# Optimization experiments

Hardware: AMD Instinct MI355X
Metric: run time of the kernel (lower is better)

Reference implementation:

```python
import jax, jax.numpy as jnp
import numpy as np

BETA = 0.25


def setup_inputs() -> dict:
    key = jax.random.key(0)
    k1, k2 = jax.random.split(key)
    x = jax.random.normal(k1, (64, 32, 32, 64), dtype=jnp.float32)
    # codebook stored as [embedding_dim, num_embeddings], as in the layer
    embeddings = jax.random.normal(k2, (64, 1024), dtype=jnp.float32) * 0.05
    return {"x": x, "embeddings": embeddings}


def reference(x, embeddings):
    input_shape = x.shape
    d = embeddings.shape[0]
    flat = x.reshape(-1, d)  # [N, D]

    sim = flat @ embeddings  # [N, K]
    distances = (
        jnp.sum(flat ** 2, axis=1, keepdims=True)
        + jnp.sum(embeddings ** 2, axis=0)
        - 2.0 * sim
    )
    encoding_indices = jnp.argmin(distances, axis=1)  # [N]

    # one_hot @ embeddings.T is mathematically a gather of codebook rows
    quantized = jnp.take(embeddings.T, encoding_indices, axis=0)  # [N, D]
    quantized = quantized.reshape(input_shape)

    commitment_loss = jnp.mean((jax.lax.stop_gradient(quantized) - x) ** 2)
    codebook_loss = jnp.mean((quantized - jax.lax.stop_gradient(x)) ** 2)
    loss = BETA * commitment_loss + codebook_loss

    # straight-through estimator
    quantized_st = x + jax.lax.stop_gradient(quantized - x)
    return quantized_st, loss
```

## Files before the change

kernel.cpp:

```cpp
#include <hip/hip_runtime.h>

#define D 64
#define K 1024
#define NPTS 65536
#define OUT_ELEMS (NPTS * D)
#define PAD4 17

typedef __bf16 bf16x8 __attribute__((ext_vector_type(8)));
typedef float  f32x4  __attribute__((ext_vector_type(4)));


static __device__ __forceinline__ void split1(float v, __bf16& h, __bf16& mid,
                                              __bf16& lo) {
    h = (__bf16)v;
    const float fh = (float)h;
    const float r1 = v - fh;
    mid = (__bf16)r1;
    const float fm = (float)mid;
    lo = (__bf16)(r1 - fm);
}

__global__ __launch_bounds__(256) void vq_prep(const float* __restrict__ emb,
                                               float* __restrict__ eT,
                                               float* __restrict__ enorm_h,
                                               __bf16* __restrict__ ebh,
                                               __bf16* __restrict__ ebm,
                                               __bf16* __restrict__ ebl,
                                               float* __restrict__ loss_out) {
    __shared__ float tile[64][65];
    const int t    = threadIdx.x;
    const int lane = t & 63;
    const int quad = t >> 6;
    const int k0   = blockIdx.x * 64;

#pragma unroll
    for (int i = 0; i < 16; ++i) {
        const int d = i * 4 + quad;
        tile[d][lane] = emb[d * K + k0 + lane];
    }
    __syncthreads();

    const int kk = t >> 2, c = t & 3;
    const int krow = k0 + kk;
#pragma unroll
    for (int j = 0; j < 16; ++j) {
        const int d = c * 16 + j;
        const float v = tile[d][kk];
        const int idx = krow * D + d;
        eT[idx] = v;
        __bf16 h, mid, lo;
        split1(v, h, mid, lo);
        ebh[idx] = h; ebm[idx] = mid; ebl[idx] = lo;
    }

    if (t < 64) {
        float s = __fmul_rn(tile[0][t], tile[0][t]);
        for (int dd = 1; dd < D; ++dd)
            s = __fadd_rn(s, __fmul_rn(tile[dd][t], tile[dd][t]));
        enorm_h[k0 + t] = 0.5f * s;
    }
    if (blockIdx.x == 0 && t == 0) *loss_out = 0.0f;
}

static __device__ __forceinline__ float sq8(float a, float b, float c, float d,
                                            float e, float f, float g, float h) {
    float r = __fmul_rn(a, a);
    r = __fadd_rn(r, __fmul_rn(b, b));
    r = __fadd_rn(r, __fmul_rn(c, c));
    r = __fadd_rn(r, __fmul_rn(d, d));
    r = __fadd_rn(r, __fmul_rn(e, e));
    r = __fadd_rn(r, __fmul_rn(f, f));
    r = __fadd_rn(r, __fmul_rn(g, g));
    r = __fadd_rn(r, __fmul_rn(h, h));
    return r;
}

#define PINF(v) asm volatile("" : "+v"(v))

#define MFMA(A, B, C) C = __builtin_amdgcn_mfma_f32_16x16x32_bf16(A, B, C, 0, 0, 0)

#define MKFRAG(FH, FM, FL, U0, U1) {                      \
    __bf16 h_, m_, l_;                                    \
    split1(U0.x, h_, m_, l_); FH[0]=h_; FM[0]=m_; FL[0]=l_; \
    split1(U0.y, h_, m_, l_); FH[1]=h_; FM[1]=m_; FL[1]=l_; \
    split1(U0.z, h_, m_, l_); FH[2]=h_; FM[2]=m_; FL[2]=l_; \
    split1(U0.w, h_, m_, l_); FH[3]=h_; FM[3]=m_; FL[3]=l_; \
    split1(U1.x, h_, m_, l_); FH[4]=h_; FM[4]=m_; FL[4]=l_; \
    split1(U1.y, h_, m_, l_); FH[5]=h_; FM[5]=m_; FL[5]=l_; \
    split1(U1.z, h_, m_, l_); FH[6]=h_; FM[6]=m_; FL[6]=l_; \
    split1(U1.w, h_, m_, l_); FH[7]=h_; FM[7]=m_; FL[7]=l_; }

static __device__ __forceinline__ void cp16(const void* gptr, void* lptr) {
    __builtin_amdgcn_global_load_lds(
        (const __attribute__((address_space(1))) void*)gptr,
        (__attribute__((address_space(3))) void*)lptr, 16, 0, 0);
}

__global__ __launch_bounds__(512, 4) void vq_main(const float* __restrict__ x,
        const float* __restrict__ eT, const float* __restrict__ enorm_h,
        const __bf16* __restrict__ ebh, const __bf16* __restrict__ ebm,
        const __bf16* __restrict__ ebl,
        float* __restrict__ out, float* __restrict__ loss_out) {
    __shared__ __align__(16) char smem[51712];
    float*  rpart = (float*)(smem + 12288);
    int*    swin  = (int*)(smem + 16384);
    float*  skey  = (float*)(smem + 16896);
    int*    sct   = (int*)(smem + 25088);
    float4* slab  = (float4*)(smem + 16896);

    const int t     = threadIdx.x;
    const int lane  = t & 63;
    const int w     = t >> 6;
    const int m     = lane & 15;
    const int quad  = lane >> 4;
    const int pbase = blockIdx.x * 128 + w * 16;

    const int n0   = lane >> 3;
    const int jj   = lane & 7;
    const int soff = n0 * 128 + (((jj - n0) & 7) << 4);
    const char* gsA = (w < 2) ? (const char*)ebh
                    : (w < 4) ? (const char*)ebm : (const char*)ebl;
    const int   IA  = w & 1;
    const int   dA  = (w >> 1) * 2048 + IA * 1024;
    const int   sA  = soff + IA * 1024;

    const int o0 = (m * 8 + ((quad + m) & 7)) * 16;
    const int o1 = (m * 8 + ((4 + quad + m) & 7)) * 16;

    if (w < 6) cp16(gsA + sA, smem + dA);

    bf16x8 Ah0, Am0, Al0, Ah1, Am1, Al1;
#define LOADA(HH, FH, FM, FL) {                                            \
    const float* px = x + ((size_t)(pbase + m)) * D + HH * 32 + quad * 8;  \
    const float4 u0 = *(const float4*)px;                                  \
    const float4 u1 = *(const float4*)(px + 4);                            \
    rpart[(w * 16 + m) * 8 + (HH * 4 + quad)] =                            \
        sq8(u0.x, u0.y, u0.z, u0.w, u1.x, u1.y, u1.z, u1.w);               \
    MKFRAG(FH, FM, FL, u0, u1); }
    LOADA(0, Ah0, Am0, Al0)
    LOADA(1, Ah1, Am1, Al1)
#undef LOADA
    PINF(Ah0); PINF(Am0); PINF(Al0); PINF(Ah1); PINF(Am1); PINF(Al1);

    const float FINF = 3.402823466e38f;
    float bk0 = FINF, bk1 = FINF, bk2 = FINF, bk3 = FINF;
    int   bc0 = 0, bc1 = 0, bc2 = 0, bc3 = 0;

#define TILE_BODY(BBOFF, CT, PRET, PREOFF) {                               \
    __syncthreads();   \
    if (w < 6) cp16(gsA + (size_t)(PRET) * 2048 + sA, smem + (PREOFF) + dA); \
    const char* bb = smem + (BBOFF);                                       \
    const bf16x8 Bh0 = *(const bf16x8*)(bb + o0);                          \
    const bf16x8 Bh1 = *(const bf16x8*)(bb + o1);                          \
    const bf16x8 Bm0 = *(const bf16x8*)(bb + 2048 + o0);                   \
    const bf16x8 Bm1 = *(const bf16x8*)(bb + 2048 + o1);                   \
    const bf16x8 Bl0 = *(const bf16x8*)(bb + 4096 + o0);                   \
    const bf16x8 Bl1 = *(const bf16x8*)(bb + 4096 + o1);                   \
    const float enh = enorm_h[(CT) * 16 + m];                              \
    f32x4 ca = {0.f,0.f,0.f,0.f}, cb = {0.f,0.f,0.f,0.f};                  \
    MFMA(Ah0, Bh0, ca); MFMA(Ah1, Bh1, cb);                        \
    MFMA(Am0, Bh0, ca); MFMA(Am1, Bh1, cb);                        \
    MFMA(Ah0, Bm0, ca); MFMA(Ah1, Bm1, cb);                        \
    MFMA(Am0, Bm0, ca); MFMA(Am1, Bm1, cb);                        \
    MFMA(Ah0, Bl0, ca); MFMA(Ah1, Bl1, cb);                        \
    MFMA(Al0, Bh0, ca); MFMA(Al1, Bh1, cb);                        \
    const f32x4 c0 = ca + cb;                                              \
    { const float kv = enh - c0[0]; if (kv < bk0) { bk0 = kv; bc0 = (CT); } } \
    { const float kv = enh - c0[1]; if (kv < bk1) { bk1 = kv; bc1 = (CT); } } \
    { const float kv = enh - c0[2]; if (kv < bk2) { bk2 = kv; bc2 = (CT); } } \
    { const float kv = enh - c0[3]; if (kv < bk3) { bk3 = kv; bc3 = (CT); } } }

    for (int j = 0; j < 32; ++j) {
        const int ct0 = 2 * j;
        const int ct1 = 2 * j + 1;
        const int tp2 = (2 * j + 2) & 63;
        TILE_BODY(0,    ct0, ct1, 6144)
        TILE_BODY(6144, ct1, tp2, 0)
    }
#undef TILE_BODY

#define PUTC(REG, BK, BC) {                                       \
    const int ploc = w * 16 + quad * 4 + REG;                     \
    skey[ploc * 16 + m] = BK; sct[ploc * 16 + m] = BC; }
    PUTC(0, bk0, bc0) PUTC(1, bk1, bc1) PUTC(2, bk2, bc2) PUTC(3, bk3, bc3)
#undef PUTC
    __syncthreads();

    if (t < 128) {
        const int p = t;
        const float* rp = rpart + p * 8;
        const float A = ((rp[0] + rp[1]) + (rp[2] + rp[3])) +
                        ((rp[4] + rp[5]) + (rp[6] + rp[7]));
        float fb = FINF;
        int   fi = 0;
#pragma unroll
        for (int c = 0; c < 16; ++c) {
            const float kv = skey[p * 16 + c];
            const int   iv = sct[p * 16 + c] * 16 + c;
            if (kv < fb || (kv == fb && iv < fi)) { fb = kv; fi = iv; }
        }
        swin[p] = fi;
        float lp = fmaf(2.0f, fb, A);
#pragma unroll
        for (int off = 32; off > 0; off >>= 1) lp += __shfl_down(lp, off, 64);
        if (lane == 0) atomicAdd(loss_out, lp * (1.25f / (float)OUT_ELEMS));
    }
    __syncthreads();

    {
        const int p = t >> 2, c = t & 3;
        const int fi = swin[p];
        const float4* qr = (const float4*)(eT + (size_t)fi * D) + c * 4;
        float4* dst = slab + p * PAD4 + c * 4;
#pragma unroll
        for (int j = 0; j < 4; ++j) dst[j] = qr[j];
    }
    __syncthreads();
    float4* og = (float4*)out + (size_t)blockIdx.x * 2048;
#pragma unroll
    for (int s = 0; s < 4; ++s) {
        const int f = s * 512 + t;
        og[f] = slab[(f >> 4) * PAD4 + (f & 15)];
    }
}

extern "C" void kernel_launch(void* const* d_in, const int* in_sizes, int n_in,
                              void* d_out, int out_size, void* d_ws, size_t ws_size,
                              hipStream_t stream) {
    const float* x   = (const float*)d_in[0];
    const float* emb = (const float*)d_in[1];
    float* out       = (float*)d_out;
    char*  ws        = (char*)d_ws;
    float*  eT       = (float*)ws;
    float*  enorm_h  = (float*)(ws + 262144);
    __bf16* ebh      = (__bf16*)(ws + 266240);
    __bf16* ebm      = (__bf16*)(ws + 397312);
    __bf16* ebl      = (__bf16*)(ws + 528384);
    float* loss_out  = out + OUT_ELEMS;

    vq_prep<<<dim3(K / 64), dim3(256), 0, stream>>>(emb, eT, enorm_h, ebh, ebm,
                                                    ebl, loss_out);
    vq_main<<<dim3(NPTS / 128), dim3(512), 0, stream>>>(x, eT, enorm_h, ebh,
                                                        ebm, ebl, out, loss_out);
}
```

Measured before the change: 122.5 us.

## Switch 3-way bf16 split to scaled 2-way fp16 split with codebook-half wave split

Replaces the three-term bf16 decomposition (six MFMAs per tile per 16 points) with an fp16 high part plus a residual scaled by 4096, so three MFMA products are needed instead of six. Work is also regrouped: each wave now holds A fragments for 32 points and scans half of the codebook, which doubles B-fragment reuse per LDS read. The final argmin merges 32 partial candidates per point instead of 16. fp16's narrower exponent range and the scaled residual could change tie-breaking or accuracy for inputs with unusual magnitudes.

```diff
diff --git a/kernel.cpp b/kernel.cpp
--- a/kernel.cpp
+++ b/kernel.cpp
@@ -6,26 +6,24 @@
 #define OUT_ELEMS (NPTS * D)
 #define PAD4 17
 
-typedef __bf16 bf16x8 __attribute__((ext_vector_type(8)));
-typedef float  f32x4  __attribute__((ext_vector_type(4)));
-
-
-static __device__ __forceinline__ void split1(float v, __bf16& h, __bf16& mid,
-                                              __bf16& lo) {
-    h = (__bf16)v;
-    const float fh = (float)h;
-    const float r1 = v - fh;
-    mid = (__bf16)r1;
-    const float fm = (float)mid;
-    lo = (__bf16)(r1 - fm);
+typedef _Float16 f16x8 __attribute__((ext_vector_type(8)));
+typedef float    f32x4 __attribute__((ext_vector_type(4)));
+
+#define SCL  4096.0f
+#define ISCL 0.000244140625f
+
+
+static __device__ __forceinline__ void split16(float v, _Float16& h, _Float16& ls) {
+    h = (_Float16)v;
+    const float r = (v - (float)h) * SCL;
+    ls = (_Float16)r;
 }
 
 __global__ __launch_bounds__(256) void vq_prep(const float* __restrict__ emb,
                                                float* __restrict__ eT,
                                                float* __restrict__ enorm_h,
-                                               __bf16* __restrict__ ebh,
-                                               __bf16* __restrict__ ebm,
-                                               __bf16* __restrict__ ebl,
+                                               _Float16* __restrict__ eh,
+                                               _Float16* __restrict__ els,
                                                float* __restrict__ loss_out) {
     __shared__ float tile[64][65];
     const int t    = threadIdx.x;
@@ -48,9 +46,9 @@
         const float v = tile[d][kk];
         const int idx = krow * D + d;
         eT[idx] = v;
-        __bf16 h, mid, lo;
-        split1(v, h, mid, lo);
-        ebh[idx] = h; ebm[idx] = mid; ebl[idx] = lo;
+        _Float16 h, ls;
+        split16(v, h, ls);
+        eh[idx] = h; els[idx] = ls;
     }
 
     if (t < 64) {
@@ -77,18 +75,18 @@
 
 #define PINF(v) asm volatile("" : "+v"(v))
 
-#define MFMA(A, B, C) C = __builtin_amdgcn_mfma_f32_16x16x32_bf16(A, B, C, 0, 0, 0)
-
-#define MKFRAG(FH, FM, FL, U0, U1) {                      \
-    __bf16 h_, m_, l_;                                    \
-    split1(U0.x, h_, m_, l_); FH[0]=h_; FM[0]=m_; FL[0]=l_; \
-    split1(U0.y, h_, m_, l_); FH[1]=h_; FM[1]=m_; FL[1]=l_; \
-    split1(U0.z, h_, m_, l_); FH[2]=h_; FM[2]=m_; FL[2]=l_; \
-    split1(U0.w, h_, m_, l_); FH[3]=h_; FM[3]=m_; FL[3]=l_; \
-    split1(U1.x, h_, m_, l_); FH[4]=h_; FM[4]=m_; FL[4]=l_; \
-    split1(U1.y, h_, m_, l_); FH[5]=h_; FM[5]=m_; FL[5]=l_; \
-    split1(U1.z, h_, m_, l_); FH[6]=h_; FM[6]=m_; FL[6]=l_; \
-    split1(U1.w, h_, m_, l_); FH[7]=h_; FM[7]=m_; FL[7]=l_; }
+#define MFMA(A, B, C) C = __builtin_amdgcn_mfma_f32_16x16x32_f16(A, B, C, 0, 0, 0)
+
+#define MKFRAG16(FH, FS, U0, U1) {                        \
+    _Float16 h_, s_;                                      \
+    split16(U0.x, h_, s_); FH[0]=h_; FS[0]=s_;            \
+    split16(U0.y, h_, s_); FH[1]=h_; FS[1]=s_;            \
+    split16(U0.z, h_, s_); FH[2]=h_; FS[2]=s_;            \
+    split16(U0.w, h_, s_); FH[3]=h_; FS[3]=s_;            \
+    split16(U1.x, h_, s_); FH[4]=h_; FS[4]=s_;            \
+    split16(U1.y, h_, s_); FH[5]=h_; FS[5]=s_;            \
+    split16(U1.z, h_, s_); FH[6]=h_; FS[6]=s_;            \
+    split16(U1.w, h_, s_); FH[7]=h_; FS[7]=s_; }
 
 static __device__ __forceinline__ void cp16(const void* gptr, void* lptr) {
     __builtin_amdgcn_global_load_lds(
@@ -98,91 +96,108 @@
 
 __global__ __launch_bounds__(512, 4) void vq_main(const float* __restrict__ x,
         const float* __restrict__ eT, const float* __restrict__ enorm_h,
-        const __bf16* __restrict__ ebh, const __bf16* __restrict__ ebm,
-        const __bf16* __restrict__ ebl,
+        const _Float16* __restrict__ eh, const _Float16* __restrict__ els,
         float* __restrict__ out, float* __restrict__ loss_out) {
-    __shared__ __align__(16) char smem[51712];
-    float*  rpart = (float*)(smem + 12288);
-    int*    swin  = (int*)(smem + 16384);
-    float*  skey  = (float*)(smem + 16896);
-    int*    sct   = (int*)(smem + 25088);
-    float4* slab  = (float4*)(smem + 16896);
+    __shared__ __align__(16) char smem[55808];
+    float*  rpart = (float*)(smem + 16384);
+    int*    swin  = (int*)(smem + 20480);
+    float*  skey  = (float*)(smem + 20992);
+    int*    sct   = (int*)(smem + 37376);
+    float4* slab  = (float4*)(smem + 20992);
 
     const int t     = threadIdx.x;
     const int lane  = t & 63;
     const int w     = t >> 6;
     const int m     = lane & 15;
     const int quad  = lane >> 4;
-    const int pbase = blockIdx.x * 128 + w * 16;
+    const int g     = w >> 1;
+    const int h     = w & 1;
+    const int pbase = blockIdx.x * 128 + g * 32;
 
     const int n0   = lane >> 3;
     const int jj   = lane & 7;
     const int soff = n0 * 128 + (((jj - n0) & 7) << 4);
-    const char* gsA = (w < 2) ? (const char*)ebh
-                    : (w < 4) ? (const char*)ebm : (const char*)ebl;
-    const int   IA  = w & 1;
-    const int   dA  = (w >> 1) * 2048 + IA * 1024;
-    const int   sA  = soff + IA * 1024;
+    const int hs   = w >> 2;
+    const char* gsrc = ((w >> 1) & 1) ? (const char*)els : (const char*)eh;
+    const char* gsb  = gsrc + (w & 1) * 1024 + soff;
+    const int   dA   = hs * 4096 + ((w >> 1) & 1) * 2048 + (w & 1) * 1024;
 
     const int o0 = (m * 8 + ((quad + m) & 7)) * 16;
     const int o1 = (m * 8 + ((4 + quad + m) & 7)) * 16;
 
-    if (w < 6) cp16(gsA + sA, smem + dA);
-
-    bf16x8 Ah0, Am0, Al0, Ah1, Am1, Al1;
-#define LOADA(HH, FH, FM, FL) {                                            \
-    const float* px = x + ((size_t)(pbase + m)) * D + HH * 32 + quad * 8;  \
+    cp16(gsb + (size_t)(hs * 32) * 2048, smem + dA);
+
+    f16x8 Ah00, As00, Ah01, As01;
+    f16x8 Ah10, As10, Ah11, As11;
+#define LOADA(TT, HH, FH, FS) {                                            \
+    const float* px = x + ((size_t)(pbase + TT * 16 + m)) * D + HH * 32 + quad * 8; \
     const float4 u0 = *(const float4*)px;                                  \
     const float4 u1 = *(const float4*)(px + 4);                            \
-    rpart[(w * 16 + m) * 8 + (HH * 4 + quad)] =                            \
-        sq8(u0.x, u0.y, u0.z, u0.w, u1.x, u1.y, u1.z, u1.w);               \
-    MKFRAG(FH, FM, FL, u0, u1); }
-    LOADA(0, Ah0, Am0, Al0)
-    LOADA(1, Ah1, Am1, Al1)
+    if (h == 0)                                                            \
+        rpart[(g * 32 + TT * 16 + m) * 8 + (HH * 4 + quad)] =              \
+            sq8(u0.x, u0.y, u0.z, u0.w, u1.x, u1.y, u1.z, u1.w);           \
+    MKFRAG16(FH, FS, u0, u1); }
+    LOADA(0, 0, Ah00, As00)
+    LOADA(0, 1, Ah01, As01)
+    LOADA(1, 0, Ah10, As10)
+    LOADA(1, 1, Ah11, As11)
 #undef LOADA
-    PINF(Ah0); PINF(Am0); PINF(Al0); PINF(Ah1); PINF(Am1); PINF(Al1);
+    PINF(Ah00); PINF(As00); PINF(Ah01); PINF(As01);
+    PINF(Ah10); PINF(As10); PINF(Ah11); PINF(As11);
 
     const float FINF = 3.402823466e38f;
-    float bk0 = FINF, bk1 = FINF, bk2 = FINF, bk3 = FINF;
-    int   bc0 = 0, bc1 = 0, bc2 = 0, bc3 = 0;
+    float bk00 = FINF, bk01 = FINF, bk02 = FINF, bk03 = FINF;
+    float bk10 = FINF, bk11 = FINF, bk12 = FINF, bk13 = FINF;
+    int   bc00 = 0, bc01 = 0, bc02 = 0, bc03 = 0;
+    int   bc10 = 0, bc11 = 0, bc12 = 0, bc13 = 0;
 
 #define TILE_BODY(BBOFF, CT, PRET, PREOFF) {                               \
-    __syncthreads();   \
-    if (w < 6) cp16(gsA + (size_t)(PRET) * 2048 + sA, smem + (PREOFF) + dA); \
-    const char* bb = smem + (BBOFF);                                       \
-    const bf16x8 Bh0 = *(const bf16x8*)(bb + o0);                          \
-    const bf16x8 Bh1 = *(const bf16x8*)(bb + o1);                          \
-    const bf16x8 Bm0 = *(const bf16x8*)(bb + 2048 + o0);                   \
-    const bf16x8 Bm1 = *(const bf16x8*)(bb + 2048 + o1);                   \
-    const bf16x8 Bl0 = *(const bf16x8*)(bb + 4096 + o0);                   \
-    const bf16x8 Bl1 = *(const bf16x8*)(bb + 4096 + o1);                   \
-    const float enh = enorm_h[(CT) * 16 + m];                              \
-    f32x4 ca = {0.f,0.f,0.f,0.f}, cb = {0.f,0.f,0.f,0.f};                  \
-    MFMA(Ah0, Bh0, ca); MFMA(Ah1, Bh1, cb);                        \
-    MFMA(Am0, Bh0, ca); MFMA(Am1, Bh1, cb);                        \
-    MFMA(Ah0, Bm0, ca); MFMA(Ah1, Bm1, cb);                        \
-    MFMA(Am0, Bm0, ca); MFMA(Am1, Bm1, cb);                        \
-    MFMA(Ah0, Bl0, ca); MFMA(Ah1, Bl1, cb);                        \
-    MFMA(Al0, Bh0, ca); MFMA(Al1, Bh1, cb);                        \
-    const f32x4 c0 = ca + cb;                                              \
-    { const float kv = enh - c0[0]; if (kv < bk0) { bk0 = kv; bc0 = (CT); } } \
-    { const float kv = enh - c0[1]; if (kv < bk1) { bk1 = kv; bc1 = (CT); } } \
-    { const float kv = enh - c0[2]; if (kv < bk2) { bk2 = kv; bc2 = (CT); } } \
-    { const float kv = enh - c0[3]; if (kv < bk3) { bk3 = kv; bc3 = (CT); } } }
-
-    for (int j = 0; j < 32; ++j) {
+    __syncthreads();     \
+    cp16(gsb + (size_t)(hs * 32 + (PRET)) * 2048, smem + (PREOFF) + dA);   \
+    const char* bb = smem + (BBOFF) + h * 4096;                            \
+    const f16x8 Bh0 = *(const f16x8*)(bb + o0);                            \
+    const f16x8 Bh1 = *(const f16x8*)(bb + o1);                            \
+    const f16x8 Bs0 = *(const f16x8*)(bb + 2048 + o0);                     \
+    const f16x8 Bs1 = *(const f16x8*)(bb + 2048 + o1);                     \
+    const float enh = enorm_h[h * 512 + (CT) * 16 + m];                    \
+    f32x4 m0a = {0.f,0.f,0.f,0.f}, m0b = {0.f,0.f,0.f,0.f};                \
+    f32x4 c0a = {0.f,0.f,0.f,0.f}, c0b = {0.f,0.f,0.f,0.f};                \
+    f32x4 m1a = {0.f,0.f,0.f,0.f}, m1b = {0.f,0.f,0.f,0.f};                \
+    f32x4 c1a = {0.f,0.f,0.f,0.f}, c1b = {0.f,0.f,0.f,0.f};                \
+    MFMA(Ah00, Bh0, m0a); MFMA(Ah10, Bh0, m1a);           \
+    MFMA(Ah01, Bh1, m0b); MFMA(Ah11, Bh1, m1b);           \
+    MFMA(As00, Bh0, c0a); MFMA(As10, Bh0, c1a);                \
+    MFMA(As01, Bh1, c0b); MFMA(As11, Bh1, c1b);                            \
+    MFMA(Ah00, Bs0, c0a); MFMA(Ah10, Bs0, c1a);                \
+    MFMA(Ah01, Bs1, c0b); MFMA(Ah11, Bs1, c1b);                            \
+    const f32x4 d0 = (m0a + m0b) + ISCL * (c0a + c0b);                     \
+    const f32x4 d1 = (m1a + m1b) + ISCL * (c1a + c1b);                     \
+    { const float kv = enh - d0[0]; if (kv < bk00) { bk00 = kv; bc00 = (CT); } } \
+    { const float kv = enh - d0[1]; if (kv < bk01) { bk01 = kv; bc01 = (CT); } } \
+    { const float kv = enh - d0[2]; if (kv < bk02) { bk02 = kv; bc02 = (CT); } } \
+    { const float kv = enh - d0[3]; if (kv < bk03) { bk03 = kv; bc03 = (CT); } } \
+    { const float kv = enh - d1[0]; if (kv < bk10) { bk10 = kv; bc10 = (CT); } } \
+    { const float kv = enh - d1[1]; if (kv < bk11) { bk11 = kv; bc11 = (CT); } } \
+    { const float kv = enh - d1[2]; if (kv < bk12) { bk12 = kv; bc12 = (CT); } } \
+    { const float kv = enh - d1[3]; if (kv < bk13) { bk13 = kv; bc13 = (CT); } } }
+
+    for (int j = 0; j < 16; ++j) {
         const int ct0 = 2 * j;
         const int ct1 = 2 * j + 1;
-        const int tp2 = (2 * j + 2) & 63;
-        TILE_BODY(0,    ct0, ct1, 6144)
-        TILE_BODY(6144, ct1, tp2, 0)
+        const int tp2 = (2 * j + 2) & 31;
+        TILE_BODY(0,    ct0, ct1, 8192)
+        TILE_BODY(8192, ct1, tp2, 0)
     }
 #undef TILE_BODY
 
-#define PUTC(REG, BK, BC) {                                       \
-    const int ploc = w * 16 + quad * 4 + REG;                     \
-    skey[ploc * 16 + m] = BK; sct[ploc * 16 + m] = BC; }
-    PUTC(0, bk0, bc0) PUTC(1, bk1, bc1) PUTC(2, bk2, bc2) PUTC(3, bk3, bc3)
+#define PUTC(TT, REG, BK, BC) {                                   \
+    const int ploc = g * 32 + TT * 16 + quad * 4 + REG;           \
+    skey[ploc * 32 + h * 16 + m] = BK;                            \
+    sct [ploc * 32 + h * 16 + m] = BC; }
+    PUTC(0, 0, bk00, bc00) PUTC(0, 1, bk01, bc01)
+    PUTC(0, 2, bk02, bc02) PUTC(0, 3, bk03, bc03)
+    PUTC(1, 0, bk10, bc10) PUTC(1, 1, bk11, bc11)
+    PUTC(1, 2, bk12, bc12) PUTC(1, 3, bk13, bc13)
 #undef PUTC
     __syncthreads();
 
@@ -194,9 +209,9 @@
         float fb = FINF;
         int   fi = 0;
 #pragma unroll
-        for (int c = 0; c < 16; ++c) {
-            const float kv = skey[p * 16 + c];
-            const int   iv = sct[p * 16 + c] * 16 + c;
+        for (int c = 0; c < 32; ++c) {
+            const float kv = skey[p * 32 + c];
+            const int   iv = (c >> 4) * 512 + sct[p * 32 + c] * 16 + (c & 15);
             if (kv < fb || (kv == fb && iv < fi)) { fb = kv; fi = iv; }
         }
         swin[p] = fi;
@@ -231,15 +246,14 @@
     const float* emb = (const float*)d_in[1];
     float* out       = (float*)d_out;
     char*  ws        = (char*)d_ws;
-    float*  eT       = (float*)ws;
-    float*  enorm_h  = (float*)(ws + 262144);
-    __bf16* ebh      = (__bf16*)(ws + 266240);
-    __bf16* ebm      = (__bf16*)(ws + 397312);
-    __bf16* ebl      = (__bf16*)(ws + 528384);
-    float* loss_out  = out + OUT_ELEMS;
-
-    vq_prep<<<dim3(K / 64), dim3(256), 0, stream>>>(emb, eT, enorm_h, ebh, ebm,
-                                                    ebl, loss_out);
-    vq_main<<<dim3(NPTS / 128), dim3(512), 0, stream>>>(x, eT, enorm_h, ebh,
-                                                        ebm, ebl, out, loss_out);
-}
+    float*    eT      = (float*)ws;
+    float*    enorm_h = (float*)(ws + 262144);
+    _Float16* eh      = (_Float16*)(ws + 266240);
+    _Float16* els     = (_Float16*)(ws + 397312);
+    float* loss_out   = out + OUT_ELEMS;
+
+    vq_prep<<<dim3(K / 64), dim3(256), 0, stream>>>(emb, eT, enorm_h, eh, els,
+                                                    loss_out);
+    vq_main<<<dim3(NPTS / 128), dim3(512), 0, stream>>>(x, eT, enorm_h, eh,
+                                                        els, out, loss_out);
+}
```

New measurement: 113.9 us. -7.0%, faster.
